# Kernel optimization log

Hardware: AMD Instinct MI355X
Metric: run time of the kernel (lower is better)

Reference implementation:

```python
import jax, jax.numpy as jnp
import numpy as np

S, B, C = 7, 2, 20
EPS = 1e-6
LAMBDA_COORD = 5.0
LAMBDA_NOOBJ = 0.5


def setup_inputs() -> dict:
    key = jax.random.key(0)
    k1, k2 = jax.random.split(key)
    N = 16384
    p = jax.random.uniform(k1, (N, S, S, B * 5 + C), dtype=jnp.float32)
    a = jax.random.uniform(k2, (N, S, S, B * 5 + C), dtype=jnp.float32)
    return {"p": p, "a": a}


def _attr(t, i):
    # i-th attribute of each of the B boxes: channels C+i, C+i+5, ... -> [N,S,S,B]
    return t[..., C + i::5]


def _coords(t):
    x, y, w, h = _attr(t, 0), _attr(t, 1), _attr(t, 2), _attr(t, 3)
    tl = jnp.stack((x - w / 2.0, y - h / 2.0), axis=-1)  # [N,S,S,B,2]
    br = jnp.stack((x + w / 2.0, y + h / 2.0), axis=-1)
    return tl, br


def _sse(x, y):
    return jnp.sum((x - y) ** 2)


def reference(p, a):
    # pairwise IoU between predicted boxes (axis 3) and target boxes (axis 4)
    p_tl, p_br = _coords(p)
    a_tl, a_br = _coords(a)
    tl = jnp.maximum(p_tl[:, :, :, :, None, :], a_tl[:, :, :, None, :, :])  # [N,S,S,B,B,2]
    br = jnp.minimum(p_br[:, :, :, :, None, :], a_br[:, :, :, None, :, :])
    sides = jnp.clip(br - tl, 0.0)
    inter = sides[..., 0] * sides[..., 1]  # [N,S,S,B,B]
    p_area = (_attr(p, 2) * _attr(p, 3))[:, :, :, :, None]
    a_area = (_attr(a, 2) * _attr(a, 3))[:, :, :, None, :]
    union = p_area + a_area - inter
    zero_union = union == 0.0
    iou = jnp.where(zero_union, 0.0, inter) / jnp.where(zero_union, EPS, union)
    max_iou = jnp.max(iou, axis=-1)  # [N,S,S,B]

    obj_i = (_attr(a, 4) > 0.0)[..., 0:1]  # [N,S,S,1]
    responsible = jnp.argmax(max_iou, axis=-1, keepdims=True) == jnp.arange(B)  # [N,S,S,B]
    obj_ij = (obj_i & responsible).astype(p.dtype)
    noobj_ij = 1.0 - obj_ij

    loss_x = _sse(obj_ij * _attr(a, 0), obj_ij * _attr(p, 0))
    loss_y = _sse(obj_ij * _attr(a, 1), obj_ij * _attr(p, 1))
    loss_w = _sse(obj_ij * jnp.sign(_attr(a, 2)) * jnp.sqrt(_attr(a, 2) + EPS),
                  obj_ij * jnp.sign(_attr(p, 2)) * jnp.sqrt(_attr(p, 2) + EPS))
    loss_h = _sse(obj_ij * jnp.sign(_attr(a, 3)) * jnp.sqrt(_attr(a, 3) + EPS),
                  obj_ij * jnp.sign(_attr(p, 3)) * jnp.sqrt(_attr(p, 3) + EPS))
    loss_conf_obj = _sse(obj_ij * obj_ij, obj_ij * _attr(p, 4))
    loss_conf_noobj = _sse(noobj_ij * obj_ij, noobj_ij * _attr(p, 4))
    obj_if = obj_i.astype(p.dtype)
    cls_loss = _sse(obj_if * p[..., 5 * B:], obj_if * a[..., 5 * B:])

    return (LAMBDA_COORD * (loss_x + loss_y + loss_w + loss_h)
            + loss_conf_obj + LAMBDA_NOOBJ * loss_conf_noobj + cls_loss)
```

## Files before the change

kernel.cpp:

```cpp
#include <hip/hip_runtime.h>


#define CH       30
#define EPSL     1e-6f
#define TPB      256
#define WAVES    (TPB / 64)
#define CSTRIDE  22
#define WTILE    (64 * CSTRIDE)

__device__ __forceinline__ float sgnf(float x) {
    return (x > 0.0f) ? 1.0f : ((x < 0.0f) ? -1.0f : 0.0f);
}

__global__ __launch_bounds__(TPB, 6) void yolo_loss_kernel(const float* __restrict__ p,
                                                           const float* __restrict__ a,
                                                           float* __restrict__ out,
                                                           long long n_cells) {
    __shared__ __align__(16) float sbuf[WAVES * WTILE];
    __shared__ float wsum[WAVES];

    const int tid  = threadIdx.x;
    const int wave = tid >> 6;
    const int lane = tid & 63;

    const long long wave_cell0 = (long long)blockIdx.x * TPB + wave * 64;
    int nc_wave = (int)min((long long)64, n_cells - wave_cell0);
    if (nc_wave < 0) nc_wave = 0;

    const char* pb = (const char*)p + wave_cell0 * 120LL;
    const char* ab = (const char*)a + wave_cell0 * 120LL;
    float* wbuf = &sbuf[wave * WTILE];

    float2 rp[10], ra[10];
    int cc[10], ss[10];
#pragma unroll
    for (int k = 0; k < 10; ++k) {
        const int i = lane + 64 * k;
        const int c = i / 10;
        const int s = i - 10 * c;
        cc[k] = c; ss[k] = s;
        const int off = c * 120 + 40 + 8 * s;
        if (c < nc_wave) rp[k] = *(const float2*)(pb + off);
    }
#pragma unroll
    for (int k = 0; k < 10; ++k) {
        const int off = cc[k] * 120 + 40 + 8 * ss[k];
        if (cc[k] < nc_wave) ra[k] = *(const float2*)(ab + off);
    }

#pragma unroll
    for (int k = 0; k < 10; ++k)
        if (cc[k] < nc_wave)
            *(float2*)&wbuf[cc[k] * CSTRIDE + 2 * ss[k]] = rp[k];
    __syncthreads();

    float pd[20];
#pragma unroll
    for (int s = 0; s < 10; ++s) {
        const float2 v = *(const float2*)&wbuf[lane * CSTRIDE + 2 * s];
        pd[2 * s] = v.x; pd[2 * s + 1] = v.y;
    }
    __syncthreads();

#pragma unroll
    for (int k = 0; k < 10; ++k)
        if (cc[k] < nc_wave)
            *(float2*)&wbuf[cc[k] * CSTRIDE + 2 * ss[k]] = ra[k];
    __syncthreads();

    float ad[20];
#pragma unroll
    for (int s = 0; s < 10; ++s) {
        const float2 v = *(const float2*)&wbuf[lane * CSTRIDE + 2 * s];
        ad[2 * s] = v.x; ad[2 * s + 1] = v.y;
    }

    float lsum = 0.0f;
    if (lane < nc_wave) {
        float pxv[2], pyv[2], pwv[2], phv[2], pcv[2];
        float axv[2], ayv[2], awv[2], ahv[2];
#pragma unroll
        for (int b = 0; b < 2; ++b) {
            pxv[b] = pd[10 + 5 * b]; pyv[b] = pd[11 + 5 * b];
            pwv[b] = pd[12 + 5 * b]; phv[b] = pd[13 + 5 * b];
            pcv[b] = pd[14 + 5 * b];
            axv[b] = ad[10 + 5 * b]; ayv[b] = ad[11 + 5 * b];
            awv[b] = ad[12 + 5 * b]; ahv[b] = ad[13 + 5 * b];
        }
        const bool obj = ad[14] > 0.0f;

        float miou[2];
#pragma unroll
        for (int pb2 = 0; pb2 < 2; ++pb2) {
            const float p_tlx = pxv[pb2] - 0.5f * pwv[pb2];
            const float p_tly = pyv[pb2] - 0.5f * phv[pb2];
            const float p_brx = pxv[pb2] + 0.5f * pwv[pb2];
            const float p_bry = pyv[pb2] + 0.5f * phv[pb2];
            const float p_area = pwv[pb2] * phv[pb2];
            float best = -3.4e38f;
#pragma unroll
            for (int ab2 = 0; ab2 < 2; ++ab2) {
                const float a_tlx = axv[ab2] - 0.5f * awv[ab2];
                const float a_tly = ayv[ab2] - 0.5f * ahv[ab2];
                const float a_brx = axv[ab2] + 0.5f * awv[ab2];
                const float a_bry = ayv[ab2] + 0.5f * ahv[ab2];
                float sx = fminf(p_brx, a_brx) - fmaxf(p_tlx, a_tlx);
                float sy = fminf(p_bry, a_bry) - fmaxf(p_tly, a_tly);
                sx = fmaxf(sx, 0.0f);
                sy = fmaxf(sy, 0.0f);
                const float inter = sx * sy;
                const float uni = p_area + awv[ab2] * ahv[ab2] - inter;
                const float iou = (uni == 0.0f) ? 0.0f : (inter / uni);
                best = fmaxf(best, iou);
            }
            miou[pb2] = best;
        }
        const int resp = (miou[1] > miou[0]) ? 1 : 0;

#pragma unroll
        for (int b = 0; b < 2; ++b) {
            const bool oij = obj && (b == resp);
            if (oij) {
                const float dx = axv[b] - pxv[b];
                const float dy = ayv[b] - pyv[b];
                const float dw = sgnf(awv[b]) * sqrtf(awv[b] + EPSL) - sgnf(pwv[b]) * sqrtf(pwv[b] + EPSL);
                const float dh = sgnf(ahv[b]) * sqrtf(ahv[b] + EPSL) - sgnf(phv[b]) * sqrtf(phv[b] + EPSL);
                const float dc = 1.0f - pcv[b];
                lsum += 5.0f * (dx * dx + dy * dy + dw * dw + dh * dh) + dc * dc;
            } else {
                lsum += 0.5f * pcv[b] * pcv[b];
            }
        }

        if (obj) {
#pragma unroll
            for (int k = 0; k < 20; ++k) {
                const float d = pd[k] - ad[k];
                lsum += d * d;
            }
        }
    }

    float v = lsum;
#pragma unroll
    for (int off = 32; off > 0; off >>= 1)
        v += __shfl_down(v, off, 64);
    if (lane == 0) wsum[wave] = v;
    __syncthreads();
    if (tid == 0) {
        float t = 0.0f;
#pragma unroll
        for (int w = 0; w < WAVES; ++w) t += wsum[w];
        atomicAdd(out, t);
    }
}

extern "C" void kernel_launch(void* const* d_in, const int* in_sizes, int n_in,
                              void* d_out, int out_size, void* d_ws, size_t ws_size,
                              hipStream_t stream) {
    const float* p = (const float*)d_in[0];
    const float* a = (const float*)d_in[1];
    float* out = (float*)d_out;

    const long long n_cells = (long long)in_sizes[0] / CH;
    const int grid = (int)((n_cells + TPB - 1) / TPB);

    hipMemsetAsync(d_out, 0, sizeof(float), stream);
    yolo_loss_kernel<<<grid, TPB, 0, stream>>>(p, a, out, n_cells);
}
```

Measured before the change: 206.0 us.

## Use persistent waves with register double-buffered tile loads

Turns the one-tile-per-wave kernel into a persistent grid of 784 blocks. Each wave strides over 64-cell tiles and prefetches the next tile's p and a slices into registers while it computes the current one. The LDS staging buffer is split into separate p and a halves, which drops the intra-wave __syncthreads between the transposes. The goal is to hide global-load latency and cut block launch overhead. The cost is roughly double the register footprint for the in-flight tiles, and the occupancy hint has been removed.

```diff
diff --git a/kernel.cpp b/kernel.cpp
--- a/kernel.cpp
+++ b/kernel.cpp
@@ -12,71 +12,43 @@
     return (x > 0.0f) ? 1.0f : ((x < 0.0f) ? -1.0f : 0.0f);
 }
 
-__global__ __launch_bounds__(TPB, 6) void yolo_loss_kernel(const float* __restrict__ p,
-                                                           const float* __restrict__ a,
-                                                           float* __restrict__ out,
-                                                           long long n_cells) {
-    __shared__ __align__(16) float sbuf[WAVES * WTILE];
-    __shared__ float wsum[WAVES];
-
-    const int tid  = threadIdx.x;
-    const int wave = tid >> 6;
-    const int lane = tid & 63;
-
-    const long long wave_cell0 = (long long)blockIdx.x * TPB + wave * 64;
-    int nc_wave = (int)min((long long)64, n_cells - wave_cell0);
-    if (nc_wave < 0) nc_wave = 0;
-
-    const char* pb = (const char*)p + wave_cell0 * 120LL;
-    const char* ab = (const char*)a + wave_cell0 * 120LL;
-    float* wbuf = &sbuf[wave * WTILE];
-
-    float2 rp[10], ra[10];
-    int cc[10], ss[10];
-#pragma unroll
-    for (int k = 0; k < 10; ++k) {
-        const int i = lane + 64 * k;
-        const int c = i / 10;
-        const int s = i - 10 * c;
-        cc[k] = c; ss[k] = s;
-        const int off = c * 120 + 40 + 8 * s;
-        if (c < nc_wave) rp[k] = *(const float2*)(pb + off);
-    }
-#pragma unroll
-    for (int k = 0; k < 10; ++k) {
-        const int off = cc[k] * 120 + 40 + 8 * ss[k];
-        if (cc[k] < nc_wave) ra[k] = *(const float2*)(ab + off);
-    }
-
-#pragma unroll
-    for (int k = 0; k < 10; ++k)
-        if (cc[k] < nc_wave)
-            *(float2*)&wbuf[cc[k] * CSTRIDE + 2 * ss[k]] = rp[k];
-    __syncthreads();
-
-    float pd[20];
+__device__ __forceinline__ void load_tile(const char* pb, const char* ab,
+                                          const int* offs, const int* cc, int nc,
+                                          float2* rp, float2* ra) {
+#pragma unroll
+    for (int k = 0; k < 10; ++k)
+        if (cc[k] < nc) rp[k] = *(const float2*)(pb + offs[k]);
+#pragma unroll
+    for (int k = 0; k < 10; ++k)
+        if (cc[k] < nc) ra[k] = *(const float2*)(ab + offs[k]);
+}
+
+__device__ __forceinline__ float compute_tile(float* wbuf, int lane,
+                                              const int* cc, const int* ss, int nc,
+                                              const float2* rp, const float2* ra) {
+    float* pbuf = wbuf;
+    float* abuf = wbuf + WTILE;
+#pragma unroll
+    for (int k = 0; k < 10; ++k)
+        if (cc[k] < nc) *(float2*)&pbuf[cc[k] * CSTRIDE + 2 * ss[k]] = rp[k];
+#pragma unroll
+    for (int k = 0; k < 10; ++k)
+        if (cc[k] < nc) *(float2*)&abuf[cc[k] * CSTRIDE + 2 * ss[k]] = ra[k];
+
+    float pd[20], ad[20];
 #pragma unroll
     for (int s = 0; s < 10; ++s) {
-        const float2 v = *(const float2*)&wbuf[lane * CSTRIDE + 2 * s];
+        const float2 v = *(const float2*)&pbuf[lane * CSTRIDE + 2 * s];
         pd[2 * s] = v.x; pd[2 * s + 1] = v.y;
     }
-    __syncthreads();
-
-#pragma unroll
-    for (int k = 0; k < 10; ++k)
-        if (cc[k] < nc_wave)
-            *(float2*)&wbuf[cc[k] * CSTRIDE + 2 * ss[k]] = ra[k];
-    __syncthreads();
-
-    float ad[20];
 #pragma unroll
     for (int s = 0; s < 10; ++s) {
-        const float2 v = *(const float2*)&wbuf[lane * CSTRIDE + 2 * s];
+        const float2 v = *(const float2*)&abuf[lane * CSTRIDE + 2 * s];
         ad[2 * s] = v.x; ad[2 * s + 1] = v.y;
     }
 
     float lsum = 0.0f;
-    if (lane < nc_wave) {
+    if (lane < nc) {
         float pxv[2], pyv[2], pwv[2], phv[2], pcv[2];
         float axv[2], ayv[2], awv[2], ahv[2];
 #pragma unroll
@@ -131,13 +103,74 @@
                 lsum += 0.5f * pcv[b] * pcv[b];
             }
         }
-
         if (obj) {
 #pragma unroll
             for (int k = 0; k < 20; ++k) {
                 const float d = pd[k] - ad[k];
                 lsum += d * d;
             }
+        }
+    }
+    return lsum;
+}
+
+__global__ __launch_bounds__(TPB) void yolo_loss_kernel(const float* __restrict__ p,
+                                                        const float* __restrict__ a,
+                                                        float* __restrict__ out,
+                                                        long long n_cells) {
+    __shared__ __align__(16) float sbuf[WAVES * 2 * WTILE];
+    __shared__ float wsum[WAVES];
+
+    const int tid  = threadIdx.x;
+    const int wave = tid >> 6;
+    const int lane = tid & 63;
+    float* wbuf = &sbuf[wave * 2 * WTILE];
+
+    int cc[10], ss[10], offs[10];
+#pragma unroll
+    for (int k = 0; k < 10; ++k) {
+        const int i = lane + 64 * k;
+        const int c = i / 10;
+        const int s = i - 10 * c;
+        cc[k] = c; ss[k] = s;
+        offs[k] = c * 120 + 40 + 8 * s;
+    }
+
+    const long long n_tiles = (n_cells + 63) >> 6;
+    const long long gwave   = (long long)blockIdx.x * WAVES + wave;
+    const long long stride  = (long long)gridDim.x * WAVES;
+
+    float lsum = 0.0f;
+
+    long long t0 = gwave;
+    float2 rpA[10], raA[10], rpB[10], raB[10];
+
+    if (t0 < n_tiles) {
+        int ncA = (int)min((long long)64, n_cells - t0 * 64);
+        load_tile((const char*)p + t0 * 7680LL, (const char*)a + t0 * 7680LL,
+                  offs, cc, ncA, rpA, raA);
+        for (;;) {
+            const long long t1 = t0 + stride;
+            const bool have1 = t1 < n_tiles;
+            int ncB = 0;
+            if (have1) {
+                ncB = (int)min((long long)64, n_cells - t1 * 64);
+                load_tile((const char*)p + t1 * 7680LL, (const char*)a + t1 * 7680LL,
+                          offs, cc, ncB, rpB, raB);
+            }
+            lsum += compute_tile(wbuf, lane, cc, ss, ncA, rpA, raA);
+            if (!have1) break;
+
+            const long long t2 = t1 + stride;
+            const bool have2 = t2 < n_tiles;
+            if (have2) {
+                ncA = (int)min((long long)64, n_cells - t2 * 64);
+                load_tile((const char*)p + t2 * 7680LL, (const char*)a + t2 * 7680LL,
+                          offs, cc, ncA, rpA, raA);
+            }
+            lsum += compute_tile(wbuf, lane, cc, ss, ncB, rpB, raB);
+            if (!have2) break;
+            t0 = t2;
         }
     }
 
@@ -163,7 +196,7 @@
     float* out = (float*)d_out;
 
     const long long n_cells = (long long)in_sizes[0] / CH;
-    const int grid = (int)((n_cells + TPB - 1) / TPB);
+    const int grid = 784;
 
     hipMemsetAsync(d_out, 0, sizeof(float), stream);
     yolo_loss_kernel<<<grid, TPB, 0, stream>>>(p, a, out, n_cells);
```

Result: slower. 214.1 us (+4.0%).

## Convert to persistent grid-stride loop over 64-cell wave tiles without block barriers

Applied to the files above, without the earlier changes.

Launches a fixed grid where each wave loops over multiple 64-cell tiles, staging p and a through its private shared-memory slice. Block-wide __syncthreads are removed since each wave only touches its own LDS region, and the occupancy hint in launch_bounds is dropped. This aims to cut barrier stalls, block launch overhead and the number of atomics. It relies on intra-wave ordering of LDS accesses without explicit barriers, and the fixed grid size is hard-coded.

```diff
diff --git a/kernel.cpp b/kernel.cpp
--- a/kernel.cpp
+++ b/kernel.cpp
@@ -12,131 +12,125 @@
     return (x > 0.0f) ? 1.0f : ((x < 0.0f) ? -1.0f : 0.0f);
 }
 
-__global__ __launch_bounds__(TPB, 6) void yolo_loss_kernel(const float* __restrict__ p,
-                                                           const float* __restrict__ a,
-                                                           float* __restrict__ out,
-                                                           long long n_cells) {
+__global__ __launch_bounds__(TPB) void yolo_loss_kernel(const float* __restrict__ p,
+                                                        const float* __restrict__ a,
+                                                        float* __restrict__ out,
+                                                        long long n_cells) {
     __shared__ __align__(16) float sbuf[WAVES * WTILE];
     __shared__ float wsum[WAVES];
 
     const int tid  = threadIdx.x;
     const int wave = tid >> 6;
     const int lane = tid & 63;
-
-    const long long wave_cell0 = (long long)blockIdx.x * TPB + wave * 64;
-    int nc_wave = (int)min((long long)64, n_cells - wave_cell0);
-    if (nc_wave < 0) nc_wave = 0;
-
-    const char* pb = (const char*)p + wave_cell0 * 120LL;
-    const char* ab = (const char*)a + wave_cell0 * 120LL;
     float* wbuf = &sbuf[wave * WTILE];
 
-    float2 rp[10], ra[10];
-    int cc[10], ss[10];
+    int cc[10], ss[10], offs[10];
 #pragma unroll
     for (int k = 0; k < 10; ++k) {
         const int i = lane + 64 * k;
         const int c = i / 10;
         const int s = i - 10 * c;
         cc[k] = c; ss[k] = s;
-        const int off = c * 120 + 40 + 8 * s;
-        if (c < nc_wave) rp[k] = *(const float2*)(pb + off);
-    }
-#pragma unroll
-    for (int k = 0; k < 10; ++k) {
-        const int off = cc[k] * 120 + 40 + 8 * ss[k];
-        if (cc[k] < nc_wave) ra[k] = *(const float2*)(ab + off);
+        offs[k] = c * 120 + 40 + 8 * s;
     }
 
+    const long long n_tiles = (n_cells + 63) >> 6;
+    const long long stride  = (long long)gridDim.x * WAVES;
+
+    float lsum = 0.0f;
+
+    for (long long t = (long long)blockIdx.x * WAVES + wave; t < n_tiles; t += stride) {
+        const char* pb = (const char*)p + t * 7680LL;
+        const char* ab = (const char*)a + t * 7680LL;
+        const int nc = (int)min((long long)64, n_cells - t * 64);
+
+        float2 rp[10], ra[10];
 #pragma unroll
-    for (int k = 0; k < 10; ++k)
-        if (cc[k] < nc_wave)
-            *(float2*)&wbuf[cc[k] * CSTRIDE + 2 * ss[k]] = rp[k];
-    __syncthreads();
+        for (int k = 0; k < 10; ++k)
+            if (cc[k] < nc) rp[k] = *(const float2*)(pb + offs[k]);
+#pragma unroll
+        for (int k = 0; k < 10; ++k)
+            if (cc[k] < nc) ra[k] = *(const float2*)(ab + offs[k]);
 
-    float pd[20];
+        float pd[20], ad[20];
 #pragma unroll
-    for (int s = 0; s < 10; ++s) {
-        const float2 v = *(const float2*)&wbuf[lane * CSTRIDE + 2 * s];
-        pd[2 * s] = v.x; pd[2 * s + 1] = v.y;
-    }
-    __syncthreads();
+        for (int k = 0; k < 10; ++k)
+            if (cc[k] < nc) *(float2*)&wbuf[cc[k] * CSTRIDE + 2 * ss[k]] = rp[k];
+#pragma unroll
+        for (int s = 0; s < 10; ++s) {
+            const float2 v = *(const float2*)&wbuf[lane * CSTRIDE + 2 * s];
+            pd[2 * s] = v.x; pd[2 * s + 1] = v.y;
+        }
+#pragma unroll
+        for (int k = 0; k < 10; ++k)
+            if (cc[k] < nc) *(float2*)&wbuf[cc[k] * CSTRIDE + 2 * ss[k]] = ra[k];
+#pragma unroll
+        for (int s = 0; s < 10; ++s) {
+            const float2 v = *(const float2*)&wbuf[lane * CSTRIDE + 2 * s];
+            ad[2 * s] = v.x; ad[2 * s + 1] = v.y;
+        }
+
+        if (lane < nc) {
+            float pxv[2], pyv[2], pwv[2], phv[2], pcv[2];
+            float axv[2], ayv[2], awv[2], ahv[2];
+#pragma unroll
+            for (int b = 0; b < 2; ++b) {
+                pxv[b] = pd[10 + 5 * b]; pyv[b] = pd[11 + 5 * b];
+                pwv[b] = pd[12 + 5 * b]; phv[b] = pd[13 + 5 * b];
+                pcv[b] = pd[14 + 5 * b];
+                axv[b] = ad[10 + 5 * b]; ayv[b] = ad[11 + 5 * b];
+                awv[b] = ad[12 + 5 * b]; ahv[b] = ad[13 + 5 * b];
+            }
+            const bool obj = ad[14] > 0.0f;
+
+            float miou[2];
+#pragma unroll
+            for (int pb2 = 0; pb2 < 2; ++pb2) {
+                const float p_tlx = pxv[pb2] - 0.5f * pwv[pb2];
+                const float p_tly = pyv[pb2] - 0.5f * phv[pb2];
+                const float p_brx = pxv[pb2] + 0.5f * pwv[pb2];
+                const float p_bry = pyv[pb2] + 0.5f * phv[pb2];
+                const float p_area = pwv[pb2] * phv[pb2];
+                float best = -3.4e38f;
+#pragma unroll
+                for (int ab2 = 0; ab2 < 2; ++ab2) {
+                    const float a_tlx = axv[ab2] - 0.5f * awv[ab2];
+                    const float a_tly = ayv[ab2] - 0.5f * ahv[ab2];
+                    const float a_brx = axv[ab2] + 0.5f * awv[ab2];
+                    const float a_bry = ayv[ab2] + 0.5f * ahv[ab2];
+                    float sx = fminf(p_brx, a_brx) - fmaxf(p_tlx, a_tlx);
+                    float sy = fminf(p_bry, a_bry) - fmaxf(p_tly, a_tly);
+                    sx = fmaxf(sx, 0.0f);
+                    sy = fmaxf(sy, 0.0f);
+                    const float inter = sx * sy;
+                    const float uni = p_area + awv[ab2] * ahv[ab2] - inter;
+                    const float iou = (uni == 0.0f) ? 0.0f : (inter / uni);
+                    best = fmaxf(best, iou);
+                }
+                miou[pb2] = best;
+            }
+            const int resp = (miou[1] > miou[0]) ? 1 : 0;
 
 #pragma unroll
-    for (int k = 0; k < 10; ++k)
-        if (cc[k] < nc_wave)
-            *(float2*)&wbuf[cc[k] * CSTRIDE + 2 * ss[k]] = ra[k];
-    __syncthreads();
-
-    float ad[20];
+            for (int b = 0; b < 2; ++b) {
+                const bool oij = obj && (b == resp);
+                if (oij) {
+                    const float dx = axv[b] - pxv[b];
+                    const float dy = ayv[b] - pyv[b];
+                    const float dw = sgnf(awv[b]) * sqrtf(awv[b] + EPSL) - sgnf(pwv[b]) * sqrtf(pwv[b] + EPSL);
+                    const float dh = sgnf(ahv[b]) * sqrtf(ahv[b] + EPSL) - sgnf(phv[b]) * sqrtf(phv[b] + EPSL);
+                    const float dc = 1.0f - pcv[b];
+                    lsum += 5.0f * (dx * dx + dy * dy + dw * dw + dh * dh) + dc * dc;
+                } else {
+                    lsum += 0.5f * pcv[b] * pcv[b];
+                }
+            }
+            if (obj) {
 #pragma unroll
-    for (int s = 0; s < 10; ++s) {
-        const float2 v = *(const float2*)&wbuf[lane * CSTRIDE + 2 * s];
-        ad[2 * s] = v.x; ad[2 * s + 1] = v.y;
-    }
-
-    float lsum = 0.0f;
-    if (lane < nc_wave) {
-        float pxv[2], pyv[2], pwv[2], phv[2], pcv[2];
-        float axv[2], ayv[2], awv[2], ahv[2];
-#pragma unroll
-        for (int b = 0; b < 2; ++b) {
-            pxv[b] = pd[10 + 5 * b]; pyv[b] = pd[11 + 5 * b];
-            pwv[b] = pd[12 + 5 * b]; phv[b] = pd[13 + 5 * b];
-            pcv[b] = pd[14 + 5 * b];
-            axv[b] = ad[10 + 5 * b]; ayv[b] = ad[11 + 5 * b];
-            awv[b] = ad[12 + 5 * b]; ahv[b] = ad[13 + 5 * b];
-        }
-        const bool obj = ad[14] > 0.0f;
-
-        float miou[2];
-#pragma unroll
-        for (int pb2 = 0; pb2 < 2; ++pb2) {
-            const float p_tlx = pxv[pb2] - 0.5f * pwv[pb2];
-            const float p_tly = pyv[pb2] - 0.5f * phv[pb2];
-            const float p_brx = pxv[pb2] + 0.5f * pwv[pb2];
-            const float p_bry = pyv[pb2] + 0.5f * phv[pb2];
-            const float p_area = pwv[pb2] * phv[pb2];
-            float best = -3.4e38f;
-#pragma unroll
-            for (int ab2 = 0; ab2 < 2; ++ab2) {
-                const float a_tlx = axv[ab2] - 0.5f * awv[ab2];
-                const float a_tly = ayv[ab2] - 0.5f * ahv[ab2];
-                const float a_brx = axv[ab2] + 0.5f * awv[ab2];
-                const float a_bry = ayv[ab2] + 0.5f * ahv[ab2];
-                float sx = fminf(p_brx, a_brx) - fmaxf(p_tlx, a_tlx);
-                float sy = fminf(p_bry, a_bry) - fmaxf(p_tly, a_tly);
-                sx = fmaxf(sx, 0.0f);
-                sy = fmaxf(sy, 0.0f);
-                const float inter = sx * sy;
-                const float uni = p_area + awv[ab2] * ahv[ab2] - inter;
-                const float iou = (uni == 0.0f) ? 0.0f : (inter / uni);
-                best = fmaxf(best, iou);
-            }
-            miou[pb2] = best;
-        }
-        const int resp = (miou[1] > miou[0]) ? 1 : 0;
-
-#pragma unroll
-        for (int b = 0; b < 2; ++b) {
-            const bool oij = obj && (b == resp);
-            if (oij) {
-                const float dx = axv[b] - pxv[b];
-                const float dy = ayv[b] - pyv[b];
-                const float dw = sgnf(awv[b]) * sqrtf(awv[b] + EPSL) - sgnf(pwv[b]) * sqrtf(pwv[b] + EPSL);
-                const float dh = sgnf(ahv[b]) * sqrtf(ahv[b] + EPSL) - sgnf(phv[b]) * sqrtf(phv[b] + EPSL);
-                const float dc = 1.0f - pcv[b];
-                lsum += 5.0f * (dx * dx + dy * dy + dw * dw + dh * dh) + dc * dc;
-            } else {
-                lsum += 0.5f * pcv[b] * pcv[b];
-            }
-        }
-
-        if (obj) {
-#pragma unroll
-            for (int k = 0; k < 20; ++k) {
-                const float d = pd[k] - ad[k];
-                lsum += d * d;
+                for (int k = 0; k < 20; ++k) {
+                    const float d = pd[k] - ad[k];
+                    lsum += d * d;
+                }
             }
         }
     }
@@ -163,7 +157,7 @@
     float* out = (float*)d_out;
 
     const long long n_cells = (long long)in_sizes[0] / CH;
-    const int grid = (int)((n_cells + TPB - 1) / TPB);
+    const int grid = 1568;
 
     hipMemsetAsync(d_out, 0, sizeof(float), stream);
     yolo_loss_kernel<<<grid, TPB, 0, stream>>>(p, a, out, n_cells);
```

New measurement: 207.4 us. Within noise of the previous version (+0.7%).
